# Performance work log

Measured on AMD Instinct MI355X. Metric: run time of the kernel, lower is better.

Reference implementation:

```python
import jax, jax.numpy as jnp
import numpy as np

TEMPERATURE = 30.0
NUM_KERNELS = 4


def setup_inputs() -> dict:
    key = jax.random.key(0)
    ks = jax.random.split(key, 7)
    B, H, W, C = 32, 56, 56, 256
    F, KH, KW, K = 256, 3, 3, NUM_KERNELS
    hidden = C // 4  # attention_reduction_ratio = 4
    x = jax.random.normal(ks[0], (B, H, W, C), dtype=jnp.float32)
    # K parallel conv kernels (HWIO layout) and biases
    fan = KH * KW * C
    kernels = jax.random.normal(ks[1], (K, KH, KW, C, F), dtype=jnp.float32) / np.sqrt(fan)
    biases = jnp.zeros((K, F), dtype=jnp.float32)
    # attention MLP: GAP -> Dense(C//4, relu) -> Dense(K)
    w1 = jax.random.normal(ks[2], (C, hidden), dtype=jnp.float32) / np.sqrt(C)
    b1 = jnp.zeros((hidden,), dtype=jnp.float32)
    w2 = jax.random.normal(ks[3], (hidden, K), dtype=jnp.float32) / np.sqrt(hidden)
    b2 = jnp.zeros((K,), dtype=jnp.float32)
    return {"x": x, "kernels": kernels, "biases": biases,
            "w1": w1, "b1": b1, "w2": w2, "b2": b2}


def reference(x, kernels, biases, w1, b1, w2, b2):
    # Attention router: GAP -> Dense(relu) -> Dense(K) -> softmax(logits / tau)
    pooled = jnp.mean(x, axis=(1, 2))                       # [B, C]
    h = jax.nn.relu(pooled @ w1 + b1)                       # [B, C//4]
    logits = h @ w2 + b2                                    # [B, K]
    attn = jax.nn.softmax(logits / TEMPERATURE, axis=-1)    # [B, K]

    # K parallel conv branches (stride 1, SAME padding, dilation 1, groups 1)
    def conv_k(w, b):
        y = jax.lax.conv_general_dilated(
            x, w, window_strides=(1, 1), padding='SAME',
            dimension_numbers=('NHWC', 'HWIO', 'NHWC'))
        return y + b                                        # [B, H, W, F]

    ys = jax.vmap(conv_k)(kernels, biases)                  # [K, B, H, W, F]
    # per-sample weighted aggregation of branch outputs
    out = jnp.einsum('kbhwf,bk->bhwf', ys, attn)            # [B, H, W, F]
    return out
```

## Files before the change

### kernel.cpp

```cpp
#include <hip/hip_runtime.h>
#include <hip/hip_bf16.h>
#include <stdint.h>

typedef __bf16 bf16_t;
typedef __bf16 bf16x4 __attribute__((ext_vector_type(4)));
typedef __bf16 bf16x8 __attribute__((ext_vector_type(8)));
typedef float floatx4 __attribute__((ext_vector_type(4)));

#define B_ 32
#define HP 58
#define WP 66

#define XPAD_OFF   0u
#define WAGG_OFF   62717952u
#define POOLED_OFF 100466688u
#define ATTN_OFF   100499456u
#define BIASAGG_OFF 100499968u

__device__ __forceinline__ void async_copy16(const void* gsrc, void* ldst) {
  __builtin_amdgcn_global_load_lds(
      (const __attribute__((address_space(1))) unsigned int*)gsrc,
      (__attribute__((address_space(3))) unsigned int*)ldst, 16, 0, 0);
}

__global__ __launch_bounds__(256)
void pad_pool(const float* __restrict__ x, bf16_t* __restrict__ xpad,
              float* __restrict__ pooled) {
  const int hp = blockIdx.x;
  const int b  = blockIdx.y;
  const int t  = threadIdx.x;
  const int c4 = (t & 63) << 2;
  const int wq = t >> 6;
  const int h  = hp - 1;
  const bool hvalid = (h >= 0) && (h < 56);
  bf16_t* dst = xpad + ((size_t)(b * 58 + hp)) * (66 * 256);
  const float* srcrow = x + ((size_t)(b * 56 + (hvalid ? h : 0))) * (56 * 256);
  floatx4 sum = {0.f, 0.f, 0.f, 0.f};
  for (int wp = wq; wp < 66; wp += 4) {
    const int w = wp - 1;
    floatx4 v = {0.f, 0.f, 0.f, 0.f};
    if (hvalid && (unsigned)w < 56u) {
      v = *(const floatx4*)(srcrow + w * 256 + c4);
      sum += v;
    }
    bf16x4 r;
#pragma unroll
    for (int j = 0; j < 4; ++j) r[j] = (bf16_t)v[j];
    *(bf16x4*)(dst + wp * 256 + c4) = r;
  }
  __shared__ floatx4 red[4][64];
  red[wq][t & 63] = sum;
  __syncthreads();
  if (hvalid && t < 64) {
    floatx4 s = red[0][t] + red[1][t] + red[2][t] + red[3][t];
#pragma unroll
    for (int j = 0; j < 4; ++j) atomicAdd(&pooled[b * 256 + t * 4 + j], s[j]);
  }
}

__global__ __launch_bounds__(256)
void router(const float* __restrict__ pooled, const float* __restrict__ w1,
            const float* __restrict__ b1, const float* __restrict__ w2,
            const float* __restrict__ b2, const float* __restrict__ biases,
            float* __restrict__ attn, float* __restrict__ biasagg) {
  __shared__ float ps[8192];
  __shared__ float w1s[16384];
  __shared__ float hs[2048];
  __shared__ float lg[128];
  __shared__ float at[128];
  const int t = threadIdx.x;
  for (int i = t; i < 8192; i += 256) ps[i] = pooled[i] * (1.0f / 3136.0f);
  for (int i = t; i < 4096; i += 256)
    *(floatx4*)&w1s[i * 4] = *(const floatx4*)&w1[i * 4];
  __syncthreads();
  for (int task = t; task < 2048; task += 256) {
    const int b = task >> 6, j = task & 63;
    const float* pb = ps + b * 256;
    float s0 = 0.f, s1 = 0.f, s2 = 0.f, s3 = 0.f;
#pragma unroll 4
    for (int c = 0; c < 256; c += 4) {
      s0 += pb[c]     * w1s[c * 64 + j];
      s1 += pb[c + 1] * w1s[(c + 1) * 64 + j];
      s2 += pb[c + 2] * w1s[(c + 2) * 64 + j];
      s3 += pb[c + 3] * w1s[(c + 3) * 64 + j];
    }
    hs[task] = fmaxf((s0 + s1) + (s2 + s3) + b1[j], 0.f);
  }
  __syncthreads();
  if (t < 128) {
    int b = t >> 2, k = t & 3;
    float s = b2[k];
    const float* hb = hs + b * 64;
#pragma unroll 4
    for (int j = 0; j < 64; ++j) s += hb[j] * w2[j * 4 + k];
    lg[t] = s * (1.0f / 30.0f);
  }
  __syncthreads();
  if (t < 32) {
    int b = t;
    float z0 = lg[b*4], z1 = lg[b*4+1], z2 = lg[b*4+2], z3 = lg[b*4+3];
    float m = fmaxf(fmaxf(z0, z1), fmaxf(z2, z3));
    float e0 = expf(z0-m), e1 = expf(z1-m), e2 = expf(z2-m), e3 = expf(z3-m);
    float inv = 1.0f / (e0 + e1 + e2 + e3);
    at[b*4] = e0*inv; at[b*4+1] = e1*inv; at[b*4+2] = e2*inv; at[b*4+3] = e3*inv;
    attn[b*4] = at[b*4]; attn[b*4+1] = at[b*4+1];
    attn[b*4+2] = at[b*4+2]; attn[b*4+3] = at[b*4+3];
  }
  __syncthreads();
  for (int i = t; i < 8192; i += 256) {
    int b = i >> 8, f = i & 255;
    biasagg[i] = at[b*4]*biases[f] + at[b*4+1]*biases[256+f]
               + at[b*4+2]*biases[512+f] + at[b*4+3]*biases[768+f];
  }
}

__global__ __launch_bounds__(256)
void wagg_kernel(const float* __restrict__ kers, const float* __restrict__ attn,
                 bf16_t* __restrict__ wagg) {
  const int lid = blockIdx.x;
  const int xcd = lid & 7;
  const int sl  = lid >> 3;
  const int c8  = sl & 7;
  const int tap = sl >> 3;
  const int b0  = xcd << 2;
  const int t   = threadIdx.x;
  __shared__ bf16_t tile[4][32 * 260];

  float a[4][4];
#pragma unroll
  for (int i = 0; i < 4; ++i)
#pragma unroll
    for (int k = 0; k < 4; ++k) a[i][k] = attn[(b0 + i) * 4 + k];

  const float* k0 = kers + ((size_t)(0 * 9 + tap)) * 65536 + (size_t)(c8 * 32) * 256;
  const float* k1 = kers + ((size_t)(1 * 9 + tap)) * 65536 + (size_t)(c8 * 32) * 256;
  const float* k2 = kers + ((size_t)(2 * 9 + tap)) * 65536 + (size_t)(c8 * 32) * 256;
  const float* k3 = kers + ((size_t)(3 * 9 + tap)) * 65536 + (size_t)(c8 * 32) * 256;

  const int fq = t & 63;
  const int cl = t >> 6;
  const int f0 = fq * 4;
#pragma unroll
  for (int pass = 0; pass < 8; ++pass) {
    const int c_local = pass * 4 + cl;
    const size_t o = (size_t)c_local * 256 + f0;
    floatx4 v0 = *(const floatx4*)(k0 + o);
    floatx4 v1 = *(const floatx4*)(k1 + o);
    floatx4 v2 = *(const floatx4*)(k2 + o);
    floatx4 v3 = *(const floatx4*)(k3 + o);
#pragma unroll
    for (int i = 0; i < 4; ++i) {
      bf16x4 r;
#pragma unroll
      for (int j = 0; j < 4; ++j)
        r[j] = (bf16_t)(a[i][0] * v0[j] + a[i][1] * v1[j] + a[i][2] * v2[j] + a[i][3] * v3[j]);
      *(bf16x4*)&tile[i][c_local * 260 + f0] = r;
    }
  }
  __syncthreads();

#pragma unroll
  for (int i = 0; i < 4; ++i) {
    bf16_t* wt = wagg + ((size_t)((b0 + i) * 9 + tap)) * 65536 + c8 * 32;
#pragma unroll
    for (int pass = 0; pass < 4; ++pass) {
      const int gi = pass * 256 + t;
      const int f  = gi >> 2;
      const int cg = gi & 3;
      bf16x8 v;
#pragma unroll
      for (int jj = 0; jj < 8; ++jj) v[jj] = tile[i][(cg * 8 + jj) * 260 + f];
      *(bf16x8*)(wt + (size_t)f * 256 + cg * 8) = v;
    }
  }
}

#define PBUF_BYTES 40960
#define BBUF_BYTES 32768

__global__ __launch_bounds__(512, 2)
void conv_mfma(const bf16_t* __restrict__ xpad, const bf16_t* __restrict__ wagg,
               const float* __restrict__ biasagg, float* __restrict__ out) {
  __shared__ char lds[2 * PBUF_BYTES + 2 * BBUF_BYTES];
  char* ldsP0 = lds;
  char* ldsP1 = lds + PBUF_BYTES;
  char* ldsB  = lds + 2 * PBUF_BYTES;

  const int lid  = blockIdx.y * 14 + blockIdx.x;
  const int nid  = (lid & 7) * 56 + (lid >> 3);
  const int b    = nid / 14;
  const int tile = nid - b * 14;
  const int h0 = (tile >> 1) * 8;
  const int w0 = (tile & 1) * 28;

  const int tid  = threadIdx.x;
  const int lane = tid & 63;
  const int wv   = tid >> 6;
  const int mg   = wv >> 2;
  const int fs   = wv & 3;
  const int l15  = lane & 15;
  const int quad = lane >> 4;
  const int n0   = fs * 64;

  const char* xb = (const char*)xpad + (size_t)b * (HP * WP * 256 * 2);
  const char* wb = (const char*)wagg + (size_t)b * (9 * 256 * 256 * 2);

  int offs[7];
#pragma unroll
  for (int mi = 0; mi < 7; ++mi) {
    int m = mg * 112 + mi * 16 + l15;
    int ty = m / 28;
    int tx = m - ty * 28;
    offs[mi] = ty * 32 + tx;
  }
  int boff[4];
#pragma unroll
  for (int ni = 0; ni < 4; ++ni) {
    int f = n0 + ni * 16 + l15;
    boff[ni] = f * 128 + ((quad ^ (f & 7)) << 4);
  }
  int sb_off[4];
#pragma unroll
  for (int ii = 0; ii < 4; ++ii) {
    int i32 = wv * 4 + ii;
    int f = i32 * 8 + (lane >> 3);
    int gsrc = (lane & 7) ^ (f & 7);
    sb_off[ii] = f * 512 + gsrc * 16;
  }
  int sp_off[5];
#pragma unroll
  for (int ii = 0; ii < 5; ++ii) {
    int i40 = wv * 5 + ii;
    int p = i40 * 8 + (lane >> 3);
    int row = p >> 5, col = p & 31;
    int gsrc = (lane & 7) ^ (p & 7);
    sp_off[ii] = ((h0 + row) * WP + (w0 + col)) * 512 + gsrc * 16;
  }

  floatx4 acc[7][4];
#pragma unroll
  for (int mi = 0; mi < 7; ++mi)
#pragma unroll
    for (int ni = 0; ni < 4; ++ni) acc[mi][ni] = (floatx4){0.f, 0.f, 0.f, 0.f};

  auto stage_patch = [&](int cq, char* pdst) {
#pragma unroll
    for (int ii = 0; ii < 5; ++ii)
      async_copy16(xb + cq * 128 + sp_off[ii], pdst + (wv * 5 + ii) * 1024);
  };
  auto stage_b = [&](int tap, int cq, int slot) {
    const char* wtb = wb + (size_t)tap * 131072 + cq * 128;
#pragma unroll
    for (int ii = 0; ii < 4; ++ii)
      async_copy16(wtb + sb_off[ii], ldsB + slot * BBUF_BYTES + (wv * 4 + ii) * 1024);
  };

  stage_patch(0, ldsP0);
  stage_b(0, 0, 0);
  asm volatile("s_waitcnt vmcnt(0)" ::: "memory");
  __builtin_amdgcn_s_barrier();
  __builtin_amdgcn_sched_barrier(0);

  bf16x8 aA[7], aB[7];
  int aoff[7];
#pragma unroll
  for (int mi = 0; mi < 7; ++mi) {
    int p = offs[mi];
    aoff[mi] = (p << 7) + ((quad ^ (p & 7)) << 4);
    aA[mi] = *(const bf16x8*)(ldsP0 + aoff[mi]);
  }

#pragma unroll 1
  for (int d = 0; d < 36; ++d) {
    const int cq  = d / 9;
    const int tap = d - cq * 9;
    const int cs  = cq & 1;
    char* pbc = cs ? ldsP1 : ldsP0;
    char* pbn = cs ? ldsP0 : ldsP1;
    const char* bc = ldsB + (d & 1) * BBUF_BYTES;
    const bool haveNext = (d < 35);

    __builtin_amdgcn_s_barrier();
    __builtin_amdgcn_sched_barrier(0);

    if (haveNext) {
      const int nt = (tap == 8) ? 0 : tap + 1;
      const int nc = (tap == 8) ? cq + 1 : cq;
      stage_b(nt, nc, (d + 1) & 1);
    }

    bf16x8 bv0 = *(const bf16x8*)(bc + boff[0]);
    bf16x8 bv1 = *(const bf16x8*)(bc + boff[1]);
    bf16x8 bv2 = *(const bf16x8*)(bc + boff[2]);
    bf16x8 bv3 = *(const bf16x8*)(bc + boff[3]);
    bf16x8 cv0 = *(const bf16x8*)(bc + (boff[0] ^ 64));
    bf16x8 cv1 = *(const bf16x8*)(bc + (boff[1] ^ 64));
    bf16x8 cv2 = *(const bf16x8*)(bc + (boff[2] ^ 64));
    bf16x8 cv3 = *(const bf16x8*)(bc + (boff[3] ^ 64));
#pragma unroll
    for (int mi = 0; mi < 7; ++mi)
      aB[mi] = *(const bf16x8*)(pbc + (aoff[mi] ^ 64));

    __builtin_amdgcn_s_setprio(1);
#pragma unroll
    for (int mi = 0; mi < 7; ++mi) {
      acc[mi][0] = __builtin_amdgcn_mfma_f32_16x16x32_bf16(aA[mi], bv0, acc[mi][0], 0, 0, 0);
      acc[mi][1] = __builtin_amdgcn_mfma_f32_16x16x32_bf16(aA[mi], bv1, acc[mi][1], 0, 0, 0);
      acc[mi][2] = __builtin_amdgcn_mfma_f32_16x16x32_bf16(aA[mi], bv2, acc[mi][2], 0, 0, 0);
      acc[mi][3] = __builtin_amdgcn_mfma_f32_16x16x32_bf16(aA[mi], bv3, acc[mi][3], 0, 0, 0);
    }
    __builtin_amdgcn_s_setprio(0);

    if (haveNext) {
      const char* npb = (tap == 8) ? pbn : pbc;
      const int ntapoff = (tap == 8) ? 0 : (((tap + 1) / 3) * 32 + ((tap + 1) % 3));
#pragma unroll
      for (int mi = 0; mi < 7; ++mi) {
        int p = offs[mi] + ntapoff;
        aoff[mi] = (p << 7) + ((quad ^ (p & 7)) << 4);
        aA[mi] = *(const bf16x8*)(npb + aoff[mi]);
      }
      if (tap == 0 && cq < 3) stage_patch(cq + 1, pbn);
    }

    __builtin_amdgcn_s_setprio(1);
#pragma unroll
    for (int mi = 0; mi < 7; ++mi) {
      acc[mi][0] = __builtin_amdgcn_mfma_f32_16x16x32_bf16(aB[mi], cv0, acc[mi][0], 0, 0, 0);
      acc[mi][1] = __builtin_amdgcn_mfma_f32_16x16x32_bf16(aB[mi], cv1, acc[mi][1], 0, 0, 0);
      acc[mi][2] = __builtin_amdgcn_mfma_f32_16x16x32_bf16(aB[mi], cv2, acc[mi][2], 0, 0, 0);
      acc[mi][3] = __builtin_amdgcn_mfma_f32_16x16x32_bf16(aB[mi], cv3, acc[mi][3], 0, 0, 0);
    }
    __builtin_amdgcn_s_setprio(0);

    if (haveNext) asm volatile("s_waitcnt vmcnt(0)" ::: "memory");
  }

  float bias[4];
#pragma unroll
  for (int ni = 0; ni < 4; ++ni) bias[ni] = biasagg[b * 256 + n0 + ni * 16 + l15];
  float* outb = out + (size_t)b * (56 * 56 * 256);
#pragma unroll
  for (int mi = 0; mi < 7; ++mi) {
#pragma unroll
    for (int rg = 0; rg < 4; ++rg) {
      int m = mg * 112 + mi * 16 + quad * 4 + rg;
      int ty = m / 28, tx = m - ty * 28;
      float* orow = outb + ((size_t)((h0 + ty) * 56) + (w0 + tx)) * 256 + n0 + l15;
#pragma unroll
      for (int ni = 0; ni < 4; ++ni) orow[ni * 16] = acc[mi][ni][rg] + bias[ni];
    }
  }
}

extern "C" void kernel_launch(void* const* d_in, const int* in_sizes, int n_in,
                              void* d_out, int out_size, void* d_ws, size_t ws_size,
                              hipStream_t stream) {
  const float* x      = (const float*)d_in[0];
  const float* kers   = (const float*)d_in[1];
  const float* biases = (const float*)d_in[2];
  const float* w1     = (const float*)d_in[3];
  const float* b1     = (const float*)d_in[4];
  const float* w2     = (const float*)d_in[5];
  const float* b2     = (const float*)d_in[6];
  float* outp = (float*)d_out;
  char* ws = (char*)d_ws;

  bf16_t* xpad   = (bf16_t*)(ws + XPAD_OFF);
  bf16_t* wagg   = (bf16_t*)(ws + WAGG_OFF);
  float* pooled  = (float*)(ws + POOLED_OFF);
  float* attn    = (float*)(ws + ATTN_OFF);
  float* biasagg = (float*)(ws + BIASAGG_OFF);

  hipMemsetAsync(pooled, 0, 32 * 256 * sizeof(float), stream);
  pad_pool<<<dim3(58, 32), 256, 0, stream>>>(x, xpad, pooled);
  router<<<1, 256, 0, stream>>>(pooled, w1, b1, w2, b2, biases, attn, biasagg);
  wagg_kernel<<<dim3(576), 256, 0, stream>>>(kers, attn, wagg);
  conv_mfma<<<dim3(14, 32), 512, 0, stream>>>(xpad, wagg, biasagg, outp);
}
```

Measured before the change: 357.0 us.

## Load aggregated weights directly into registers and drop per-tap LDS barriers

The per-sample weight fragments now go straight from global memory into registers, with a one-step register prefetch (Bcur/Bnext), instead of being staged through double-buffered LDS. That removes the 64 KB weight LDS buffers and the workgroup barrier on every tap iteration. Barriers are kept only at channel-quarter boundaries, where the input patch buffer switches. In exchange, each wave issues its own uncoalesced 16-byte global loads with no reuse across waves, adds vector register pressure that could hurt occupancy, and the patch prefetch is now issued at the start of each quarter.

```diff
diff --git a/kernel.cpp b/kernel.cpp
--- a/kernel.cpp
+++ b/kernel.cpp
@@ -176,15 +176,13 @@
 }
 
 #define PBUF_BYTES 40960
-#define BBUF_BYTES 32768
 
 __global__ __launch_bounds__(512, 2)
 void conv_mfma(const bf16_t* __restrict__ xpad, const bf16_t* __restrict__ wagg,
                const float* __restrict__ biasagg, float* __restrict__ out) {
-  __shared__ char lds[2 * PBUF_BYTES + 2 * BBUF_BYTES];
+  __shared__ char lds[2 * PBUF_BYTES];
   char* ldsP0 = lds;
   char* ldsP1 = lds + PBUF_BYTES;
-  char* ldsB  = lds + 2 * PBUF_BYTES;
 
   const int lid  = blockIdx.y * 14 + blockIdx.x;
   const int nid  = (lid & 7) * 56 + (lid >> 3);
@@ -213,20 +211,7 @@
     int tx = m - ty * 28;
     offs[mi] = ty * 32 + tx;
   }
-  int boff[4];
-#pragma unroll
-  for (int ni = 0; ni < 4; ++ni) {
-    int f = n0 + ni * 16 + l15;
-    boff[ni] = f * 128 + ((quad ^ (f & 7)) << 4);
-  }
-  int sb_off[4];
-#pragma unroll
-  for (int ii = 0; ii < 4; ++ii) {
-    int i32 = wv * 4 + ii;
-    int f = i32 * 8 + (lane >> 3);
-    int gsrc = (lane & 7) ^ (f & 7);
-    sb_off[ii] = f * 512 + gsrc * 16;
-  }
+  const char* bbase = wb + (size_t)(n0 + l15) * 512 + quad * 16;
   int sp_off[5];
 #pragma unroll
   for (int ii = 0; ii < 5; ++ii) {
@@ -248,55 +233,60 @@
     for (int ii = 0; ii < 5; ++ii)
       async_copy16(xb + cq * 128 + sp_off[ii], pdst + (wv * 5 + ii) * 1024);
   };
-  auto stage_b = [&](int tap, int cq, int slot) {
-    const char* wtb = wb + (size_t)tap * 131072 + cq * 128;
-#pragma unroll
-    for (int ii = 0; ii < 4; ++ii)
-      async_copy16(wtb + sb_off[ii], ldsB + slot * BBUF_BYTES + (wv * 4 + ii) * 1024);
+  auto load_B = [&](int cq, int tap, bf16x8* dst) {
+    const char* base = bbase + (size_t)tap * 131072 + cq * 128;
+#pragma unroll
+    for (int ni = 0; ni < 4; ++ni) {
+      dst[ni]     = *(const bf16x8*)(base + ni * 8192);
+      dst[4 + ni] = *(const bf16x8*)(base + ni * 8192 + 64);
+    }
   };
 
   stage_patch(0, ldsP0);
-  stage_b(0, 0, 0);
   asm volatile("s_waitcnt vmcnt(0)" ::: "memory");
   __builtin_amdgcn_s_barrier();
   __builtin_amdgcn_sched_barrier(0);
 
+  bf16x8 Bcur[8], Bnext[8];
+  load_B(0, 0, Bcur);
+
   bf16x8 aA[7], aB[7];
-  int aoff[7];
-#pragma unroll
-  for (int mi = 0; mi < 7; ++mi) {
-    int p = offs[mi];
-    aoff[mi] = (p << 7) + ((quad ^ (p & 7)) << 4);
-    aA[mi] = *(const bf16x8*)(ldsP0 + aoff[mi]);
-  }
 
 #pragma unroll 1
   for (int d = 0; d < 36; ++d) {
     const int cq  = d / 9;
     const int tap = d - cq * 9;
-    const int cs  = cq & 1;
-    char* pbc = cs ? ldsP1 : ldsP0;
-    char* pbn = cs ? ldsP0 : ldsP1;
-    const char* bc = ldsB + (d & 1) * BBUF_BYTES;
+    char* pbc = (cq & 1) ? ldsP1 : ldsP0;
+    char* pbn = (cq & 1) ? ldsP0 : ldsP1;
     const bool haveNext = (d < 35);
 
-    __builtin_amdgcn_s_barrier();
-    __builtin_amdgcn_sched_barrier(0);
+    if (tap == 0 && cq < 3) stage_patch(cq + 1, pbn);
 
     if (haveNext) {
       const int nt = (tap == 8) ? 0 : tap + 1;
       const int nc = (tap == 8) ? cq + 1 : cq;
-      stage_b(nt, nc, (d + 1) & 1);
-    }
-
-    bf16x8 bv0 = *(const bf16x8*)(bc + boff[0]);
-    bf16x8 bv1 = *(const bf16x8*)(bc + boff[1]);
-    bf16x8 bv2 = *(const bf16x8*)(bc + boff[2]);
-    bf16x8 bv3 = *(const bf16x8*)(bc + boff[3]);
-    bf16x8 cv0 = *(const bf16x8*)(bc + (boff[0] ^ 64));
-    bf16x8 cv1 = *(const bf16x8*)(bc + (boff[1] ^ 64));
-    bf16x8 cv2 = *(const bf16x8*)(bc + (boff[2] ^ 64));
-    bf16x8 cv3 = *(const bf16x8*)(bc + (boff[3] ^ 64));
+      load_B(nc, nt, Bnext);
+    }
+
+    const int tapoff = (tap / 3) * 32 + (tap % 3);
+    int aoff[7];
+#pragma unroll
+    for (int mi = 0; mi < 7; ++mi) {
+      int p = offs[mi] + tapoff;
+      aoff[mi] = (p << 7) + ((quad ^ (p & 7)) << 4);
+      aA[mi] = *(const bf16x8*)(pbc + aoff[mi]);
+    }
+
+    __builtin_amdgcn_s_setprio(1);
+#pragma unroll
+    for (int mi = 0; mi < 7; ++mi) {
+      acc[mi][0] = __builtin_amdgcn_mfma_f32_16x16x32_bf16(aA[mi], Bcur[0], acc[mi][0], 0, 0, 0);
+      acc[mi][1] = __builtin_amdgcn_mfma_f32_16x16x32_bf16(aA[mi], Bcur[1], acc[mi][1], 0, 0, 0);
+      acc[mi][2] = __builtin_amdgcn_mfma_f32_16x16x32_bf16(aA[mi], Bcur[2], acc[mi][2], 0, 0, 0);
+      acc[mi][3] = __builtin_amdgcn_mfma_f32_16x16x32_bf16(aA[mi], Bcur[3], acc[mi][3], 0, 0, 0);
+    }
+    __builtin_amdgcn_s_setprio(0);
+
 #pragma unroll
     for (int mi = 0; mi < 7; ++mi)
       aB[mi] = *(const bf16x8*)(pbc + (aoff[mi] ^ 64));
@@ -304,36 +294,23 @@
     __builtin_amdgcn_s_setprio(1);
 #pragma unroll
     for (int mi = 0; mi < 7; ++mi) {
-      acc[mi][0] = __builtin_amdgcn_mfma_f32_16x16x32_bf16(aA[mi], bv0, acc[mi][0], 0, 0, 0);
-      acc[mi][1] = __builtin_amdgcn_mfma_f32_16x16x32_bf16(aA[mi], bv1, acc[mi][1], 0, 0, 0);
-      acc[mi][2] = __builtin_amdgcn_mfma_f32_16x16x32_bf16(aA[mi], bv2, acc[mi][2], 0, 0, 0);
-      acc[mi][3] = __builtin_amdgcn_mfma_f32_16x16x32_bf16(aA[mi], bv3, acc[mi][3], 0, 0, 0);
+      acc[mi][0] = __builtin_amdgcn_mfma_f32_16x16x32_bf16(aB[mi], Bcur[4], acc[mi][0], 0, 0, 0);
+      acc[mi][1] = __builtin_amdgcn_mfma_f32_16x16x32_bf16(aB[mi], Bcur[5], acc[mi][1], 0, 0, 0);
+      acc[mi][2] = __builtin_amdgcn_mfma_f32_16x16x32_bf16(aB[mi], Bcur[6], acc[mi][2], 0, 0, 0);
+      acc[mi][3] = __builtin_amdgcn_mfma_f32_16x16x32_bf16(aB[mi], Bcur[7], acc[mi][3], 0, 0, 0);
     }
     __builtin_amdgcn_s_setprio(0);
 
+    if (tap == 8 && cq < 3) {
+      asm volatile("s_waitcnt vmcnt(0)" ::: "memory");
+      __builtin_amdgcn_s_barrier();
+      __builtin_amdgcn_sched_barrier(0);
+    }
+
     if (haveNext) {
-      const char* npb = (tap == 8) ? pbn : pbc;
-      const int ntapoff = (tap == 8) ? 0 : (((tap + 1) / 3) * 32 + ((tap + 1) % 3));
-#pragma unroll
-      for (int mi = 0; mi < 7; ++mi) {
-        int p = offs[mi] + ntapoff;
-        aoff[mi] = (p << 7) + ((quad ^ (p & 7)) << 4);
-        aA[mi] = *(const bf16x8*)(npb + aoff[mi]);
-      }
-      if (tap == 0 && cq < 3) stage_patch(cq + 1, pbn);
-    }
-
-    __builtin_amdgcn_s_setprio(1);
-#pragma unroll
-    for (int mi = 0; mi < 7; ++mi) {
-      acc[mi][0] = __builtin_amdgcn_mfma_f32_16x16x32_bf16(aB[mi], cv0, acc[mi][0], 0, 0, 0);
-      acc[mi][1] = __builtin_amdgcn_mfma_f32_16x16x32_bf16(aB[mi], cv1, acc[mi][1], 0, 0, 0);
-      acc[mi][2] = __builtin_amdgcn_mfma_f32_16x16x32_bf16(aB[mi], cv2, acc[mi][2], 0, 0, 0);
-      acc[mi][3] = __builtin_amdgcn_mfma_f32_16x16x32_bf16(aB[mi], cv3, acc[mi][3], 0, 0, 0);
-    }
-    __builtin_amdgcn_s_setprio(0);
-
-    if (haveNext) asm volatile("s_waitcnt vmcnt(0)" ::: "memory");
+#pragma unroll
+      for (int i = 0; i < 8; ++i) Bcur[i] = Bnext[i];
+    }
   }
 
   float bias[4];
```

Measured after the change: 401.8 us. 1.13x slower.
